# Kernel optimization log

Hardware: AMD Instinct MI355X
Metric: run time of the kernel (lower is better)

The kernel has to match this reference:

```python
import jax, jax.numpy as jnp
import numpy as np

N_NODES = 100000
N_EDGES = 3200000
NUM_GRAPHS = 128
IN_DIM = 15
HID = 64


def setup_inputs() -> dict:
    key = jax.random.key(0)
    ks = jax.random.split(key, 12)
    x = jax.random.normal(ks[0], (N_NODES, IN_DIM), dtype=jnp.float32)
    edge_index = jax.random.randint(ks[1], (2, N_EDGES), 0, N_NODES, dtype=jnp.int64)
    batch = jnp.sort(jax.random.randint(ks[2], (N_NODES,), 0, NUM_GRAPHS, dtype=jnp.int64))
    # Glorot-style weights for the 4 GCNConv layers, zero biases (PyG default)
    def glorot(k, fan_in, fan_out):
        s = jnp.sqrt(6.0 / (fan_in + fan_out))
        return jax.random.uniform(k, (fan_in, fan_out), jnp.float32, -s, s)
    return {
        "x": x,
        "w1": glorot(ks[3], IN_DIM, HID), "b1": jnp.zeros((HID,), jnp.float32),
        "w2": glorot(ks[4], HID, HID),    "b2": jnp.zeros((HID,), jnp.float32),
        "w3": glorot(ks[5], HID, HID),    "b3": jnp.zeros((HID,), jnp.float32),
        "w4": glorot(ks[6], HID, HID),    "b4": jnp.zeros((HID,), jnp.float32),
        "edge_index": edge_index,
        "batch": batch,
    }


def _gcn_norm(edge_index, num_nodes):
    # PyG gcn_norm with add_self_loops=True: A_hat = A + I, norm = d^-1/2[src] * d^-1/2[dst]
    loops = jnp.arange(num_nodes, dtype=edge_index.dtype)
    src = jnp.concatenate([edge_index[0], loops])
    dst = jnp.concatenate([edge_index[1], loops])
    deg = jax.ops.segment_sum(jnp.ones_like(dst, dtype=jnp.float32), dst,
                              num_segments=num_nodes)
    dis = jnp.where(deg > 0, jax.lax.rsqrt(deg), 0.0)
    norm = dis[src] * dis[dst]  # [E + N]
    return src, dst, norm


def _gcn_conv(h, w, b, src, dst, norm, num_nodes):
    h = h @ w                               # linear transform first (PyG order)
    msg = h[src] * norm[:, None]            # gather + scale  [E+N, HID]
    agg = jax.ops.segment_sum(msg, dst, num_segments=num_nodes)  # scatter-add
    return agg + b


def reference(x, w1, b1, w2, b2, w3, b3, w4, b4, edge_index, batch):
    n = x.shape[0]
    src, dst, norm = _gcn_norm(edge_index, n)
    h = jax.nn.relu(_gcn_conv(x, w1, b1, src, dst, norm, n))
    h = jax.nn.relu(_gcn_conv(h, w2, b2, src, dst, norm, n))
    h = jax.nn.relu(_gcn_conv(h, w3, b3, src, dst, norm, n))
    h = jax.nn.relu(_gcn_conv(h, w4, b4, src, dst, norm, n))
    # global_mean_pool over graph ids
    sums = jax.ops.segment_sum(h, batch, num_segments=NUM_GRAPHS)
    cnts = jax.ops.segment_sum(jnp.ones((n,), jnp.float32), batch,
                               num_segments=NUM_GRAPHS)
    return sums / jnp.maximum(cnts, 1.0)[:, None]
```

## Files before the change

kernel.cpp:

```cpp
#include <hip/hip_runtime.h>
#include <hip/hip_fp16.h>

#define NN 100000
#define NE 3200000
#define NG 128
#define HID 64

#define BSH 9
#define BNODES 512
#define NBK ((NN + BNODES - 1) / BNODES)
#define CCH 4096

typedef __attribute__((ext_vector_type(2))) _Float16 half2v;
typedef __attribute__((ext_vector_type(4))) _Float16 half4v;

#if __has_builtin(__builtin_amdgcn_fdot2)
#define FDOT2(v, o, a) __builtin_amdgcn_fdot2((v), (o), (a), false)
#else
static __device__ inline float FDOT2(half2v v, half2v o, float a) {
    return a + (float)v.x * (float)o.x + (float)v.y * (float)o.y;
}
#endif

__global__ __launch_bounds__(256) void bcount_kernel(const int* __restrict__ dst,
                                                     int* __restrict__ bcnt, int E) {
    __shared__ int h[NBK];
    for (int i = threadIdx.x; i < NBK; i += 256) h[i] = 0;
    __syncthreads();
    for (int e = blockIdx.x * 256 + threadIdx.x; e < E; e += gridDim.x * 256)
        atomicAdd(&h[dst[e] >> BSH], 1);
    __syncthreads();
    for (int i = threadIdx.x; i < NBK; i += 256)
        if (h[i]) atomicAdd(&bcnt[i], h[i]);
}

__global__ __launch_bounds__(256) void bscan_kernel(const int* __restrict__ bcnt,
                                                    int* __restrict__ bbase,
                                                    int* __restrict__ bcur, int E) {
    __shared__ int s[NBK];
    int t = threadIdx.x;
    if (t < NBK) s[t] = bcnt[t];
    __syncthreads();
    if (t == 0) {
        int acc = 0;
        for (int i = 0; i < NBK; ++i) { int v = s[i]; s[i] = acc; acc += v; }
    }
    __syncthreads();
    if (t < NBK) { bbase[t] = s[t]; bcur[t] = s[t]; }
    if (t == 0) bbase[NBK] = E;
}

__global__ __launch_bounds__(256) void bscatter_kernel(const int* __restrict__ src,
                                                       const int* __restrict__ dst,
                                                       int* __restrict__ bcur,
                                                       unsigned* __restrict__ pairs,
                                                       int E) {
    __shared__ unsigned stage[CCH];
    __shared__ unsigned char bb[CCH];
    __shared__ int cnt[NBK];
    __shared__ int base[NBK];
    const int e0 = blockIdx.x * CCH;
    const int n  = min(CCH, E - e0);
    if (n <= 0) return;
    for (int i = threadIdx.x; i < NBK; i += 256) cnt[i] = 0;
    __syncthreads();
    for (int i = threadIdx.x; i < n; i += 256) {
        int s = src[e0 + i], d = dst[e0 + i];
        int b = d >> BSH;
        stage[i] = ((unsigned)(d & (BNODES - 1)) << 17) | (unsigned)s;
        bb[i] = (unsigned char)b;
        atomicAdd(&cnt[b], 1);
    }
    __syncthreads();
    for (int i = threadIdx.x; i < NBK; i += 256) {
        int c = cnt[i];
        base[i] = c ? atomicAdd(&bcur[i], c) : 0;
        cnt[i] = 0;
    }
    __syncthreads();
    for (int i = threadIdx.x; i < n; i += 256) {
        int b = bb[i];
        int pos = base[b] + atomicAdd(&cnt[b], 1);
        pairs[pos] = stage[i];
    }
}

__global__ __launch_bounds__(256) void csr_kernel(const unsigned* __restrict__ pairs,
                                                  const int* __restrict__ bbase,
                                                  int* __restrict__ rowptr,
                                                  int* __restrict__ csr_src,
                                                  float* __restrict__ dis,
                                                  int N, int E) {
    __shared__ int hist[BNODES];
    __shared__ int cur[BNODES];
    __shared__ int s[256];
    const int b     = blockIdx.x;
    const int t     = threadIdx.x;
    const int node0 = b << BSH;
    const int nn    = min(BNODES, N - node0);
    const int p0 = bbase[b], p1 = bbase[b + 1];

    for (int i = t; i < BNODES; i += 256) hist[i] = 0;
    __syncthreads();
    for (int i = p0 + t; i < p1; i += 256)
        atomicAdd(&hist[pairs[i] >> 17], 1);
    __syncthreads();

    int h0 = hist[2 * t], h1 = hist[2 * t + 1];
    int v = h0 + h1;
    s[t] = v;
    __syncthreads();
    for (int off = 1; off < 256; off <<= 1) {
        int u = (t >= off) ? s[t - off] : 0;
        __syncthreads();
        s[t] += u;
        __syncthreads();
    }
    int excl = s[t] - v;
    int e0 = p0 + excl;
    int e1 = e0 + h0;
    if (2 * t < nn) {
        rowptr[node0 + 2 * t] = e0;
        dis[node0 + 2 * t] = rsqrtf((float)h0 + 1.0f);
        cur[2 * t] = e0;
    }
    if (2 * t + 1 < nn) {
        rowptr[node0 + 2 * t + 1] = e1;
        dis[node0 + 2 * t + 1] = rsqrtf((float)h1 + 1.0f);
        cur[2 * t + 1] = e1;
    }
    if (b == NBK - 1 && t == 0) rowptr[N] = E;
    __syncthreads();

    for (int i = p0 + t; i < p1; i += 256) {
        unsigned p = pairs[i];
        int pos = atomicAdd(&cur[p >> 17], 1);
        csr_src[pos] = (int)(p & 0x1FFFFu);
    }
}

__global__ __launch_bounds__(256) void xprep_kernel(const float* __restrict__ x,
                                                    const float* __restrict__ dis,
                                                    __half* __restrict__ x16h, int N) {
    int gid = blockIdx.x * 256 + threadIdx.x;
    if (gid >= N * 16) return;
    int node = gid >> 4, k = gid & 15;
    float v = (k < 15) ? x[node * 15 + k] * dis[node] : 0.0f;
    x16h[gid] = __float2half(v);
}

__global__ __launch_bounds__(256) void gather16_kernel(const half4v* __restrict__ xh,
                                                       const int* __restrict__ csr_src,
                                                       const int* __restrict__ rowptr,
                                                       const float* __restrict__ dis,
                                                       float4* __restrict__ aggx, int N) {
    const int gid  = blockIdx.x * 256 + threadIdx.x;
    const int node = gid >> 2;
    if (node >= N) return;
    const int l  = threadIdx.x & 3;
    const int gb = threadIdx.x & 60;
    const int start = rowptr[node], end = rowptr[node + 1];
    const half2v ONEX = {(_Float16)1.0f, (_Float16)0.0f};
    const half2v ONEY = {(_Float16)0.0f, (_Float16)1.0f};
    float a0 = 0.0f, a1 = 0.0f, a2 = 0.0f, a3 = 0.0f;
    for (int j0 = start; j0 < end; j0 += 4) {
        int j   = j0 + l;
        int s   = (j < end) ? csr_src[j] : 0;
        int cnt = min(4, end - j0);
#pragma unroll
        for (int k = 0; k < 4; ++k) {
            int sk = __shfl(s, gb + k);
            if (k < cnt) {
                half4v v = xh[sk * 4 + l];
                half2v p0 = __builtin_shufflevector(v, v, 0, 1);
                half2v p1 = __builtin_shufflevector(v, v, 2, 3);
                a0 = FDOT2(p0, ONEX, a0);
                a1 = FDOT2(p0, ONEY, a1);
                a2 = FDOT2(p1, ONEX, a2);
                a3 = FDOT2(p1, ONEY, a3);
            }
        }
    }
    half4v sv = xh[node * 4 + l];
    half2v s0 = __builtin_shufflevector(sv, sv, 0, 1);
    half2v s1 = __builtin_shufflevector(sv, sv, 2, 3);
    a0 += (float)s0.x; a1 += (float)s0.y;
    a2 += (float)s1.x; a3 += (float)s1.y;
    float sn = dis[node];
    aggx[(size_t)node * 4 + l] = make_float4(sn * a0, sn * a1, sn * a2, sn * a3);
}

__global__ __launch_bounds__(256) void gemm12_kernel(const float* __restrict__ in,
                                                     const float* __restrict__ w1,
                                                     const float* __restrict__ b1,
                                                     const float* __restrict__ w2,
                                                     const float* __restrict__ dis,
                                                     __half* __restrict__ th_out, int N) {
    __shared__ float w1_s[16 * 64];
    __shared__ float in_s[64 * 17];
    __shared__ float w2_s[64 * 64];
    __shared__ float h_s[64 * 65];
    const int tid  = threadIdx.x;
    const int row0 = blockIdx.x * 64;
    const int rows = min(64, N - row0);

    for (int i = tid; i < 16 * 64; i += 256) w1_s[i] = (i < 15 * 64) ? w1[i] : 0.0f;
    for (int i = tid; i < 64 * 64; i += 256) w2_s[i] = w2[i];
    for (int i = tid; i < rows * 16; i += 256) {
        int r = i >> 4, k = i & 15;
        in_s[r * 17 + k] = in[(size_t)(row0 + r) * 16 + k];
    }
    __syncthreads();

    const int r  = tid & 63;
    const int cg = tid >> 6;
    {
        float acc[16];
#pragma unroll
        for (int i = 0; i < 16; ++i) acc[i] = 0.0f;
#pragma unroll
        for (int k = 0; k < 16; ++k) {
            float a = in_s[r * 17 + k];
#pragma unroll
            for (int cc = 0; cc < 16; ++cc)
                acc[cc] += a * w1_s[k * 64 + cg * 16 + cc];
        }
#pragma unroll
        for (int cc = 0; cc < 16; ++cc)
            h_s[r * 65 + cg * 16 + cc] = fmaxf(acc[cc] + b1[cg * 16 + cc], 0.0f);
    }
    __syncthreads();
    {
        const float2* w2v = reinterpret_cast<const float2*>(w2_s);
        float2 acc2[8];
#pragma unroll
        for (int i = 0; i < 8; ++i) acc2[i] = make_float2(0.0f, 0.0f);
#pragma unroll
        for (int k = 0; k < 64; ++k) {
            float a = h_s[r * 65 + k];
            const float2* wk = w2v + k * 32 + cg * 8;
#pragma unroll
            for (int i = 0; i < 8; ++i) {
                float2 wv = wk[i];
                acc2[i].x += a * wv.x;
                acc2[i].y += a * wv.y;
            }
        }
        const int row = row0 + r;
        if (row < N) {
            float sd = dis[row];
            __align__(16) __half2 hh[8];
#pragma unroll
            for (int i = 0; i < 8; ++i)
                hh[i] = __floats2half2_rn(acc2[i].x * sd, acc2[i].y * sd);
            float4* tp = reinterpret_cast<float4*>(th_out + (size_t)row * HID + cg * 16);
            tp[0] = reinterpret_cast<float4*>(hh)[0];
            tp[1] = reinterpret_cast<float4*>(hh)[1];
        }
    }
}

__global__ __launch_bounds__(256) void fusedGG_kernel(const half2v* __restrict__ th_in,
                                                      const int* __restrict__ csr_src,
                                                      const int* __restrict__ rowptr,
                                                      const float* __restrict__ dis,
                                                      const float* __restrict__ w,
                                                      const float* __restrict__ bias,
                                                      __half* __restrict__ th_out, int N) {
    __shared__ float w_s[64 * 64];
    __shared__ float r_s[8][64];
    const int tid = threadIdx.x;
    {
        const float4* wsrc = reinterpret_cast<const float4*>(w);
        float4* wdst = reinterpret_cast<float4*>(w_s);
        for (int i = tid; i < 1024; i += 256) wdst[i] = wsrc[i];
    }
    const int g    = tid >> 5;
    const int node = blockIdx.x * 8 + g;
    const int l    = tid & 31;
    const int hb   = tid & 32;
    float u0 = 0.0f, u1 = 0.0f;
    if (node < N) {
        const int start = rowptr[node], end = rowptr[node + 1];
        const half2v* tl = th_in + l;
        const half2v ONEX = {(_Float16)1.0f, (_Float16)0.0f};
        const half2v ONEY = {(_Float16)0.0f, (_Float16)1.0f};
        float ax = 0.0f, ay = 0.0f;
        for (int j0 = start; j0 < end; j0 += 32) {
            int j   = j0 + l;
            int s   = (j < end) ? csr_src[j] : 0;
            int cnt = min(32, end - j0);
            int k = 0;
            for (; k + 16 <= cnt; k += 16) {
                int sk[16];
#pragma unroll
                for (int u = 0; u < 16; ++u) sk[u] = __shfl(s, hb + k + u);
                half2v v[16];
#pragma unroll
                for (int u = 0; u < 16; ++u) v[u] = tl[sk[u] * 32];
#pragma unroll
                for (int u = 0; u < 16; ++u) {
                    ax = FDOT2(v[u], ONEX, ax);
                    ay = FDOT2(v[u], ONEY, ay);
                }
            }
            for (; k + 4 <= cnt; k += 4) {
                int s0 = __shfl(s, hb + k);
                int s1 = __shfl(s, hb + k + 1);
                int s2 = __shfl(s, hb + k + 2);
                int s3 = __shfl(s, hb + k + 3);
                half2v v0 = tl[s0 * 32];
                half2v v1 = tl[s1 * 32];
                half2v v2 = tl[s2 * 32];
                half2v v3 = tl[s3 * 32];
                ax = FDOT2(v0, ONEX, ax); ay = FDOT2(v0, ONEY, ay);
                ax = FDOT2(v1, ONEX, ax); ay = FDOT2(v1, ONEY, ay);
                ax = FDOT2(v2, ONEX, ax); ay = FDOT2(v2, ONEY, ay);
                ax = FDOT2(v3, ONEX, ax); ay = FDOT2(v3, ONEY, ay);
            }
            for (; k < cnt; ++k) {
                half2v v = tl[__shfl(s, hb + k) * 32];
                ax += (float)v.x; ay += (float)v.y;
            }
        }
        half2v self = tl[node * 32];
        ax += (float)self.x; ay += (float)self.y;
        float sn = dis[node];
        float2 bv = reinterpret_cast<const float2*>(bias)[l];
        u0 = fmaxf(sn * ax + bv.x, 0.0f);
        u1 = fmaxf(sn * ay + bv.y, 0.0f);
    }
    reinterpret_cast<float2*>(r_s[g])[l] = make_float2(u0, u1);
    __syncthreads();
    if (node < N) {
        const float2* wv = reinterpret_cast<const float2*>(w_s);
        float c0 = 0.0f, c1 = 0.0f;
#pragma unroll 8
        for (int k = 0; k < 64; ++k) {
            float u = r_s[g][k];
            float2 ww = wv[k * 32 + l];
            c0 += u * ww.x;
            c1 += u * ww.y;
        }
        float sd = dis[node];
        reinterpret_cast<__half2*>(th_out)[(size_t)node * 32 + l] =
            __floats2half2_rn(c0 * sd, c1 * sd);
    }
}

__global__ __launch_bounds__(256) void gatherh_kernel(const half2v* __restrict__ th,
                                                      const int* __restrict__ csr_src,
                                                      const int* __restrict__ rowptr,
                                                      const float* __restrict__ dis,
                                                      float* __restrict__ agg, int N) {
    const int gid  = blockIdx.x * 256 + threadIdx.x;
    const int node = gid >> 5;
    if (node >= N) return;
    const int l  = threadIdx.x & 31;
    const int hb = threadIdx.x & 32;
    const int start = rowptr[node], end = rowptr[node + 1];
    const half2v* tl = th + l;
    const half2v ONEX = {(_Float16)1.0f, (_Float16)0.0f};
    const half2v ONEY = {(_Float16)0.0f, (_Float16)1.0f};
    float ax = 0.0f, ay = 0.0f;
    for (int j0 = start; j0 < end; j0 += 32) {
        int j   = j0 + l;
        int s   = (j < end) ? csr_src[j] : 0;
        int cnt = min(32, end - j0);
        int k = 0;
        for (; k + 16 <= cnt; k += 16) {
            int sk[16];
#pragma unroll
            for (int u = 0; u < 16; ++u) sk[u] = __shfl(s, hb + k + u);
            half2v v[16];
#pragma unroll
            for (int u = 0; u < 16; ++u) v[u] = tl[sk[u] * 32];
#pragma unroll
            for (int u = 0; u < 16; ++u) {
                ax = FDOT2(v[u], ONEX, ax);
                ay = FDOT2(v[u], ONEY, ay);
            }
        }
        for (; k + 4 <= cnt; k += 4) {
            int s0 = __shfl(s, hb + k);
            int s1 = __shfl(s, hb + k + 1);
            int s2 = __shfl(s, hb + k + 2);
            int s3 = __shfl(s, hb + k + 3);
            half2v v0 = tl[s0 * 32];
            half2v v1 = tl[s1 * 32];
            half2v v2 = tl[s2 * 32];
            half2v v3 = tl[s3 * 32];
            ax = FDOT2(v0, ONEX, ax); ay = FDOT2(v0, ONEY, ay);
            ax = FDOT2(v1, ONEX, ax); ay = FDOT2(v1, ONEY, ay);
            ax = FDOT2(v2, ONEX, ax); ay = FDOT2(v2, ONEY, ay);
            ax = FDOT2(v3, ONEX, ax); ay = FDOT2(v3, ONEY, ay);
        }
        for (; k < cnt; ++k) {
            half2v v = tl[__shfl(s, hb + k) * 32];
            ax += (float)v.x; ay += (float)v.y;
        }
    }
    half2v self = tl[node * 32];
    ax += (float)self.x; ay += (float)self.y;
    float sn = dis[node];
    reinterpret_cast<float2*>(agg)[(size_t)node * 32 + l] =
        make_float2(sn * ax, sn * ay);
}

__global__ __launch_bounds__(256) void pool_kernel(const float* __restrict__ agg,
                                                   const float* __restrict__ b4,
                                                   const int* __restrict__ batch,
                                                   float* __restrict__ sums,
                                                   float* __restrict__ cnts, int N) {
    __shared__ float lsum[NG * HID];
    __shared__ float lcnt[NG];
    const int tid  = threadIdx.x;
    const int base = blockIdx.x * 256;
    const int last = min(base + 256, N) - 1;
    const int gfirst = batch[base];
    const int glast  = batch[last];
    const int span   = glast - gfirst + 1;

    for (int i = tid; i < span * HID; i += 256) lsum[i] = 0.0f;
    for (int i = tid; i < span; i += 256) lcnt[i] = 0.0f;
    __syncthreads();

    const int f = tid & 63, sub = tid >> 6;
    for (int n = base + sub; n < min(base + 256, N); n += 4) {
        int g = batch[n];
        float v = fmaxf(agg[(size_t)n * HID + f] + b4[f], 0.0f);
        atomicAdd(&lsum[(g - gfirst) * HID + f], v);
        if (f == 0) atomicAdd(&lcnt[g - gfirst], 1.0f);
    }
    __syncthreads();

    for (int i = tid; i < span * HID; i += 256)
        atomicAdd(&sums[(size_t)gfirst * HID + i], lsum[i]);
    for (int i = tid; i < span; i += 256) atomicAdd(&cnts[gfirst + i], lcnt[i]);
}

__global__ __launch_bounds__(256) void finalize_kernel(const float* __restrict__ sums,
                                                       const float* __restrict__ cnts,
                                                       float* __restrict__ out) {
    int i = blockIdx.x * 256 + threadIdx.x;
    if (i < NG * HID) out[i] = sums[i] / fmaxf(cnts[i >> 6], 1.0f);
}

extern "C" void kernel_launch(void* const* d_in, const int* in_sizes, int n_in,
                              void* d_out, int out_size, void* d_ws, size_t ws_size,
                              hipStream_t stream) {
    const float* x  = (const float*)d_in[0];
    const float* w1 = (const float*)d_in[1];
    const float* b1 = (const float*)d_in[2];
    const float* w2 = (const float*)d_in[3];
    const float* b2 = (const float*)d_in[4];
    const float* w3 = (const float*)d_in[5];
    const float* b3 = (const float*)d_in[6];
    const float* w4 = (const float*)d_in[7];
    const float* b4 = (const float*)d_in[8];
    const int* ei    = (const int*)d_in[9];
    const int* batch = (const int*)d_in[10];
    const int* src = ei;
    const int* dst = ei + NE;

    float*    AGG     = (float*)d_ws;
    __half*   thB     = (__half*)d_ws;
    __half*   thA     = (__half*)(AGG + (size_t)NN * HID);
    unsigned* pairs   = (unsigned*)(thA + (size_t)NN * HID);
    __half*   x16h    = (__half*)pairs;
    float*    aggx    = (float*)(x16h + (size_t)NN * 16);
    int*      csr_src = (int*)((char*)pairs + (size_t)NE * 4);
    int*      rowptr  = csr_src + NE;
    float*    dis     = (float*)(rowptr + NN + 1);
    int*      bcnt    = (int*)(dis + NN);
    int*      bbase   = bcnt + NBK;
    int*      bcur    = bbase + NBK + 1;
    float*    sums    = (float*)(bcur + NBK);
    float*    cnts    = sums + NG * HID;

    float* out = (float*)d_out;

    const int NB  = (NN + 255) / 256;
    const int GB  = (NN + 63) / 64;
    const int XB  = (NN * 16 + 255) / 256;
    const int OB  = (NN * 4 + 255) / 256;
    const int HB  = (NN * 32 + 255) / 256;
    const int FB  = (NN + 7) / 8;
    const int CB  = (NE + CCH - 1) / CCH;

    hipMemsetAsync(bcnt, 0, NBK * sizeof(int), stream);
    hipMemsetAsync(sums, 0, (NG * HID + NG) * sizeof(float), stream);

    bcount_kernel<<<512, 256, 0, stream>>>(dst, bcnt, NE);
    bscan_kernel<<<1, 256, 0, stream>>>(bcnt, bbase, bcur, NE);
    bscatter_kernel<<<CB, 256, 0, stream>>>(src, dst, bcur, pairs, NE);
    csr_kernel<<<NBK, 256, 0, stream>>>(pairs, bbase, rowptr, csr_src, dis, NN, NE);

    xprep_kernel<<<XB, 256, 0, stream>>>(x, dis, x16h, NN);
    gather16_kernel<<<OB, 256, 0, stream>>>((const half4v*)x16h, csr_src, rowptr, dis,
                                            (float4*)aggx, NN);
    gemm12_kernel<<<GB, 256, 0, stream>>>(aggx, w1, b1, w2, dis, thA, NN);
    fusedGG_kernel<<<FB, 256, 0, stream>>>((const half2v*)thA, csr_src, rowptr, dis,
                                           w3, b2, thB, NN);
    fusedGG_kernel<<<FB, 256, 0, stream>>>((const half2v*)thB, csr_src, rowptr, dis,
                                           w4, b3, thA, NN);
    gatherh_kernel<<<HB, 256, 0, stream>>>((const half2v*)thA, csr_src, rowptr, dis, AGG, NN);

    pool_kernel<<<NB, 256, 0, stream>>>(AGG, b4, batch, sums, cnts, NN);
    finalize_kernel<<<(NG * HID + 255) / 256, 256, 0, stream>>>(sums, cnts, out);
}
```

Baseline: 527.2 us.

## Fuse final gather with mean pooling and remap fusedGG GEMV thread layout

Merges the last-layer gather and the global mean pool into one kernel that adds bias, applies ReLU and accumulates per-graph sums in shared memory, so the fp32 AGG buffer is never written to or read back from global memory. The GEMV stage in fusedGG is remapped so each wave covers all 8 nodes for its column pairs, and the r_s shared array is padded to 66 floats to change the LDS access pattern. The fused pool relies on sorted batch ids, so each 8-node block spans at most 8 graphs, and it issues more global atomics per block than before. The workspace layout is simplified to two fp16 buffers.

Result: slower. 854.9 us (+62.2%).

```diff
diff --git a/kernel.cpp b/kernel.cpp
--- a/kernel.cpp
+++ b/kernel.cpp
@@ -268,7 +268,7 @@
                                                       const float* __restrict__ bias,
                                                       __half* __restrict__ th_out, int N) {
     __shared__ float w_s[64 * 64];
-    __shared__ float r_s[8][64];
+    __shared__ float r_s[8][66];
     const int tid = threadIdx.x;
     {
         const float4* wsrc = reinterpret_cast<const float4*>(w);
@@ -330,113 +330,111 @@
         u0 = fmaxf(sn * ax + bv.x, 0.0f);
         u1 = fmaxf(sn * ay + bv.y, 0.0f);
     }
-    reinterpret_cast<float2*>(r_s[g])[l] = make_float2(u0, u1);
-    __syncthreads();
-    if (node < N) {
+    r_s[g][2 * l]     = u0;
+    r_s[g][2 * l + 1] = u1;
+    __syncthreads();
+    const int g2    = tid & 7;
+    const int cp    = tid >> 3;
+    const int node2 = blockIdx.x * 8 + g2;
+    if (node2 < N) {
         const float2* wv = reinterpret_cast<const float2*>(w_s);
         float c0 = 0.0f, c1 = 0.0f;
 #pragma unroll 8
         for (int k = 0; k < 64; ++k) {
-            float u = r_s[g][k];
-            float2 ww = wv[k * 32 + l];
+            float u = r_s[g2][k];
+            float2 ww = wv[k * 32 + cp];
             c0 += u * ww.x;
             c1 += u * ww.y;
         }
-        float sd = dis[node];
-        reinterpret_cast<__half2*>(th_out)[(size_t)node * 32 + l] =
+        float sd = dis[node2];
+        reinterpret_cast<__half2*>(th_out)[(size_t)node2 * 32 + cp] =
             __floats2half2_rn(c0 * sd, c1 * sd);
     }
 }
 
-__global__ __launch_bounds__(256) void gatherh_kernel(const half2v* __restrict__ th,
+__global__ __launch_bounds__(256) void fusedGP_kernel(const half2v* __restrict__ th,
                                                       const int* __restrict__ csr_src,
                                                       const int* __restrict__ rowptr,
                                                       const float* __restrict__ dis,
-                                                      float* __restrict__ agg, int N) {
-    const int gid  = blockIdx.x * 256 + threadIdx.x;
-    const int node = gid >> 5;
-    if (node >= N) return;
-    const int l  = threadIdx.x & 31;
-    const int hb = threadIdx.x & 32;
-    const int start = rowptr[node], end = rowptr[node + 1];
-    const half2v* tl = th + l;
-    const half2v ONEX = {(_Float16)1.0f, (_Float16)0.0f};
-    const half2v ONEY = {(_Float16)0.0f, (_Float16)1.0f};
-    float ax = 0.0f, ay = 0.0f;
-    for (int j0 = start; j0 < end; j0 += 32) {
-        int j   = j0 + l;
-        int s   = (j < end) ? csr_src[j] : 0;
-        int cnt = min(32, end - j0);
-        int k = 0;
-        for (; k + 16 <= cnt; k += 16) {
-            int sk[16];
-#pragma unroll
-            for (int u = 0; u < 16; ++u) sk[u] = __shfl(s, hb + k + u);
-            half2v v[16];
-#pragma unroll
-            for (int u = 0; u < 16; ++u) v[u] = tl[sk[u] * 32];
-#pragma unroll
-            for (int u = 0; u < 16; ++u) {
-                ax = FDOT2(v[u], ONEX, ax);
-                ay = FDOT2(v[u], ONEY, ay);
-            }
-        }
-        for (; k + 4 <= cnt; k += 4) {
-            int s0 = __shfl(s, hb + k);
-            int s1 = __shfl(s, hb + k + 1);
-            int s2 = __shfl(s, hb + k + 2);
-            int s3 = __shfl(s, hb + k + 3);
-            half2v v0 = tl[s0 * 32];
-            half2v v1 = tl[s1 * 32];
-            half2v v2 = tl[s2 * 32];
-            half2v v3 = tl[s3 * 32];
-            ax = FDOT2(v0, ONEX, ax); ay = FDOT2(v0, ONEY, ay);
-            ax = FDOT2(v1, ONEX, ax); ay = FDOT2(v1, ONEY, ay);
-            ax = FDOT2(v2, ONEX, ax); ay = FDOT2(v2, ONEY, ay);
-            ax = FDOT2(v3, ONEX, ax); ay = FDOT2(v3, ONEY, ay);
-        }
-        for (; k < cnt; ++k) {
-            half2v v = tl[__shfl(s, hb + k) * 32];
-            ax += (float)v.x; ay += (float)v.y;
-        }
-    }
-    half2v self = tl[node * 32];
-    ax += (float)self.x; ay += (float)self.y;
-    float sn = dis[node];
-    reinterpret_cast<float2*>(agg)[(size_t)node * 32 + l] =
-        make_float2(sn * ax, sn * ay);
-}
-
-__global__ __launch_bounds__(256) void pool_kernel(const float* __restrict__ agg,
-                                                   const float* __restrict__ b4,
-                                                   const int* __restrict__ batch,
-                                                   float* __restrict__ sums,
-                                                   float* __restrict__ cnts, int N) {
-    __shared__ float lsum[NG * HID];
-    __shared__ float lcnt[NG];
+                                                      const float* __restrict__ b4,
+                                                      const int* __restrict__ batch,
+                                                      float* __restrict__ sums,
+                                                      float* __restrict__ cnts, int N) {
+    __shared__ float lsum[8 * 64];
+    __shared__ int lcnt[8];
+    __shared__ int gfirst_s;
     const int tid  = threadIdx.x;
-    const int base = blockIdx.x * 256;
-    const int last = min(base + 256, N) - 1;
-    const int gfirst = batch[base];
-    const int glast  = batch[last];
-    const int span   = glast - gfirst + 1;
-
-    for (int i = tid; i < span * HID; i += 256) lsum[i] = 0.0f;
-    for (int i = tid; i < span; i += 256) lcnt[i] = 0.0f;
-    __syncthreads();
-
-    const int f = tid & 63, sub = tid >> 6;
-    for (int n = base + sub; n < min(base + 256, N); n += 4) {
-        int g = batch[n];
-        float v = fmaxf(agg[(size_t)n * HID + f] + b4[f], 0.0f);
-        atomicAdd(&lsum[(g - gfirst) * HID + f], v);
-        if (f == 0) atomicAdd(&lcnt[g - gfirst], 1.0f);
-    }
-    __syncthreads();
-
-    for (int i = tid; i < span * HID; i += 256)
-        atomicAdd(&sums[(size_t)gfirst * HID + i], lsum[i]);
-    for (int i = tid; i < span; i += 256) atomicAdd(&cnts[gfirst + i], lcnt[i]);
+    const int g    = tid >> 5;
+    const int node = blockIdx.x * 8 + g;
+    const int l    = tid & 31;
+    const int hb   = tid & 32;
+    for (int i = tid; i < 512; i += 256) lsum[i] = 0.0f;
+    if (tid < 8) lcnt[tid] = 0;
+    if (tid == 0) gfirst_s = batch[blockIdx.x * 8];
+    __syncthreads();
+
+    if (node < N) {
+        const int start = rowptr[node], end = rowptr[node + 1];
+        const half2v* tl = th + l;
+        const half2v ONEX = {(_Float16)1.0f, (_Float16)0.0f};
+        const half2v ONEY = {(_Float16)0.0f, (_Float16)1.0f};
+        float ax = 0.0f, ay = 0.0f;
+        for (int j0 = start; j0 < end; j0 += 32) {
+            int j   = j0 + l;
+            int s   = (j < end) ? csr_src[j] : 0;
+            int cnt = min(32, end - j0);
+            int k = 0;
+            for (; k + 16 <= cnt; k += 16) {
+                int sk[16];
+#pragma unroll
+                for (int u = 0; u < 16; ++u) sk[u] = __shfl(s, hb + k + u);
+                half2v v[16];
+#pragma unroll
+                for (int u = 0; u < 16; ++u) v[u] = tl[sk[u] * 32];
+#pragma unroll
+                for (int u = 0; u < 16; ++u) {
+                    ax = FDOT2(v[u], ONEX, ax);
+                    ay = FDOT2(v[u], ONEY, ay);
+                }
+            }
+            for (; k + 4 <= cnt; k += 4) {
+                int s0 = __shfl(s, hb + k);
+                int s1 = __shfl(s, hb + k + 1);
+                int s2 = __shfl(s, hb + k + 2);
+                int s3 = __shfl(s, hb + k + 3);
+                half2v v0 = tl[s0 * 32];
+                half2v v1 = tl[s1 * 32];
+                half2v v2 = tl[s2 * 32];
+                half2v v3 = tl[s3 * 32];
+                ax = FDOT2(v0, ONEX, ax); ay = FDOT2(v0, ONEY, ay);
+                ax = FDOT2(v1, ONEX, ax); ay = FDOT2(v1, ONEY, ay);
+                ax = FDOT2(v2, ONEX, ax); ay = FDOT2(v2, ONEY, ay);
+                ax = FDOT2(v3, ONEX, ax); ay = FDOT2(v3, ONEY, ay);
+            }
+            for (; k < cnt; ++k) {
+                half2v v = tl[__shfl(s, hb + k) * 32];
+                ax += (float)v.x; ay += (float)v.y;
+            }
+        }
+        half2v self = tl[node * 32];
+        ax += (float)self.x; ay += (float)self.y;
+        float sn = dis[node];
+        float2 bv = reinterpret_cast<const float2*>(b4)[l];
+        float v0 = fmaxf(sn * ax + bv.x, 0.0f);
+        float v1 = fmaxf(sn * ay + bv.y, 0.0f);
+        int grel = batch[node] - gfirst_s;
+        atomicAdd(&lsum[grel * 64 + 2 * l], v0);
+        atomicAdd(&lsum[grel * 64 + 2 * l + 1], v1);
+        if (l == 0) atomicAdd(&lcnt[grel], 1);
+    }
+    __syncthreads();
+    for (int i = tid; i < 512; i += 256) {
+        int sgi = i >> 6;
+        if (lcnt[sgi] > 0)
+            atomicAdd(&sums[(size_t)(gfirst_s + sgi) * 64 + (i & 63)], lsum[i]);
+    }
+    if (tid < 8 && lcnt[tid] > 0)
+        atomicAdd(&cnts[gfirst_s + tid], (float)lcnt[tid]);
 }
 
 __global__ __launch_bounds__(256) void finalize_kernel(const float* __restrict__ sums,
@@ -463,10 +461,9 @@
     const int* src = ei;
     const int* dst = ei + NE;
 
-    float*    AGG     = (float*)d_ws;
-    __half*   thB     = (__half*)d_ws;
-    __half*   thA     = (__half*)(AGG + (size_t)NN * HID);
-    unsigned* pairs   = (unsigned*)(thA + (size_t)NN * HID);
+    __half*   thA     = (__half*)d_ws;
+    __half*   thB     = thA + (size_t)NN * HID;
+    unsigned* pairs   = (unsigned*)(thB + (size_t)NN * HID);
     __half*   x16h    = (__half*)pairs;
     float*    aggx    = (float*)(x16h + (size_t)NN * 16);
     int*      csr_src = (int*)((char*)pairs + (size_t)NE * 4);
@@ -480,11 +477,9 @@
 
     float* out = (float*)d_out;
 
-    const int NB  = (NN + 255) / 256;
     const int GB  = (NN + 63) / 64;
     const int XB  = (NN * 16 + 255) / 256;
     const int OB  = (NN * 4 + 255) / 256;
-    const int HB  = (NN * 32 + 255) / 256;
     const int FB  = (NN + 7) / 8;
     const int CB  = (NE + CCH - 1) / CCH;
 
@@ -504,8 +499,8 @@
                                            w3, b2, thB, NN);
     fusedGG_kernel<<<FB, 256, 0, stream>>>((const half2v*)thB, csr_src, rowptr, dis,
                                            w4, b3, thA, NN);
-    gatherh_kernel<<<HB, 256, 0, stream>>>((const half2v*)thA, csr_src, rowptr, dis, AGG, NN);
-
-    pool_kernel<<<NB, 256, 0, stream>>>(AGG, b4, batch, sums, cnts, NN);
+    fusedGP_kernel<<<FB, 256, 0, stream>>>((const half2v*)thA, csr_src, rowptr, dis,
+                                           b4, batch, sums, cnts, NN);
+
     finalize_kernel<<<(NG * HID + 255) / 256, 256, 0, stream>>>(sums, cnts, out);
 }
```
